# Kernel tuning notes

Hardware: AMD Instinct MI355X
Metric: run time of the kernel (lower is better)

The kernel has to match this reference:

```python
import jax, jax.numpy as jnp
import numpy as np

SPATIAL_SHAPES = np.array([[100, 100], [50, 50], [25, 25], [13, 13]], dtype=np.int32)
EMBED, NH, NL, NP = 256, 8, 4, 4
HD = EMBED // NH  # 32


def setup_inputs() -> dict:
    key = jax.random.key(0)
    ks = jax.random.split(key, 12)
    bs, nq = 4, 4000
    nv = int((SPATIAL_SHAPES[:, 0] * SPATIAL_SHAPES[:, 1]).sum())  # 13294
    s_lin = 1.0 / np.sqrt(EMBED)  # xavier-ish scale
    s_small = 0.02                # offsets/weights heads start near init
    return {
        "query": jax.random.normal(ks[0], (bs, nq, EMBED), jnp.float32),
        "value": jax.random.normal(ks[1], (bs, nv, EMBED), jnp.float32),
        "reference_points": jax.random.uniform(ks[2], (bs, nq, NL, 2), jnp.float32),
        "spatial_shapes": jnp.asarray(SPATIAL_SHAPES),
        "W_off": jax.random.normal(ks[3], (EMBED, NH * NL * NP * 2), jnp.float32) * s_small,
        "b_off": jax.random.normal(ks[4], (NH * NL * NP * 2,), jnp.float32) * s_small,
        "W_attn": jax.random.normal(ks[5], (EMBED, NH * NL * NP), jnp.float32) * s_small,
        "b_attn": jax.random.normal(ks[6], (NH * NL * NP,), jnp.float32) * s_small,
        "W_val": jax.random.normal(ks[7], (EMBED, EMBED), jnp.float32) * s_lin,
        "b_val": jnp.zeros((EMBED,), jnp.float32),
        "W_out": jax.random.normal(ks[8], (EMBED, EMBED), jnp.float32) * s_lin,
        "b_out": jnp.zeros((EMBED,), jnp.float32),
    }


def _bilinear_sample(val_l, H, W, x, y):
    """grid_sample(mode=bilinear, padding=zeros, align_corners=False) equivalent.
    val_l: [bs, nh, H*W, hd]; x, y: [bs, nh, nq, np] pixel-space coords.
    Returns [bs, nh, nq, np, hd]."""
    x0 = jnp.floor(x)
    y0 = jnp.floor(y)
    bs, nh, nq, npts = x.shape
    out = 0.0
    for dx, dy in ((0, 0), (1, 0), (0, 1), (1, 1)):
        xi = x0 + dx
        yi = y0 + dy
        w = (1.0 - jnp.abs(x - xi)) * (1.0 - jnp.abs(y - yi))
        valid = (xi >= 0) & (xi < W) & (yi >= 0) & (yi < H)
        idx = (jnp.clip(yi, 0, H - 1) * W + jnp.clip(xi, 0, W - 1)).astype(jnp.int32)
        g = jnp.take_along_axis(val_l, idx.reshape(bs, nh, nq * npts, 1), axis=2)
        g = g.reshape(bs, nh, nq, npts, -1)
        out = out + g * (w * valid.astype(w.dtype))[..., None]
    return out


def reference(query, value, reference_points, spatial_shapes,
              W_off, b_off, W_attn, b_attn, W_val, b_val, W_out, b_out):
    shapes = np.asarray(spatial_shapes)  # static level shapes
    bs, nq, _ = query.shape
    # value projection -> per-head layout [bs, nh, nv, hd]
    v = (value @ W_val + b_val).reshape(bs, -1, NH, HD).transpose(0, 2, 1, 3)
    # sampling offsets and attention weights from query
    off = (query @ W_off + b_off).reshape(bs, nq, NH, NL, NP, 2)
    attn = jax.nn.softmax((query @ W_attn + b_attn).reshape(bs, nq, NH, NL * NP), axis=-1)
    attn = attn.reshape(bs, nq, NH, NL, NP)
    # normalized sampling locations; normalizer = (W, H) per level
    normalizer = jnp.asarray(np.stack([shapes[:, 1], shapes[:, 0]], -1), jnp.float32)
    loc = reference_points[:, :, None, :, None, :] + off / normalizer[None, None, None, :, None, :]
    out = jnp.zeros((bs, NH, nq, HD), query.dtype)
    start = 0
    for l in range(NL):
        H, W = int(shapes[l, 0]), int(shapes[l, 1])
        val_l = v[:, :, start:start + H * W, :]
        # pixel coords with align_corners=False: p = loc*size - 0.5
        x = loc[:, :, :, l, :, 0].transpose(0, 2, 1, 3) * W - 0.5  # [bs,nh,nq,np]
        y = loc[:, :, :, l, :, 1].transpose(0, 2, 1, 3) * H - 0.5
        sampled = _bilinear_sample(val_l, H, W, x, y)  # [bs,nh,nq,np,hd]
        out = out + jnp.einsum('bhqpd,bqhp->bhqd', sampled, attn[:, :, :, l, :])
        start += H * W
    out = out.transpose(0, 2, 1, 3).reshape(bs, nq, EMBED)
    return out @ W_out + b_out
```

## Files before the change

### kernel.cpp

```cpp
#include <hip/hip_runtime.h>
#include <hip/hip_bf16.h>

#define EMBED 256
#define NH 8
#define NL 4
#define NP 4
#define HD 32
#define BS 4
#define NQ 4000
#define NV 13294

using f32x4   = __attribute__((ext_vector_type(4))) float;
using bf16x8  = __attribute__((ext_vector_type(8))) short;

__device__ __forceinline__ float bf2f_lo(unsigned u) {
    union { unsigned u; float f; } x; x.u = u << 16; return x.f;
}
__device__ __forceinline__ float bf2f_hi(unsigned u) {
    union { unsigned u; float f; } x; x.u = u & 0xffff0000u; return x.f;
}
__device__ __forceinline__ unsigned short f2bf(float f) {
    union { float f; unsigned u; } x; x.f = f;
    unsigned u = x.u;
    return (unsigned short)((u + 0x7fffu + ((u >> 16) & 1u)) >> 16);
}
__device__ __forceinline__ unsigned cvtpk(float lo, float hi) {
    unsigned r;
    asm("v_cvt_pk_bf16_f32 %0, %1, %2" : "=v"(r) : "v"(lo), "v"(hi));
    return r;
}

__device__ __forceinline__ void async16(const void* g, void* l) {
    __builtin_amdgcn_global_load_lds(
        (const __attribute__((address_space(1))) void*)g,
        (__attribute__((address_space(3))) void*)l, 16, 0, 0);
}

template<int N> __device__ __forceinline__ void wait_vmcnt() {
    if constexpr (N == 0)      asm volatile("s_waitcnt vmcnt(0)" ::: "memory");
    else if constexpr (N == 2) asm volatile("s_waitcnt vmcnt(2)" ::: "memory");
    else if constexpr (N == 3) asm volatile("s_waitcnt vmcnt(3)" ::: "memory");
}

__global__ __launch_bounds__(256) void msda_prep_k(
    const float* __restrict__ W_val, const float* __restrict__ W_out,
    const float* __restrict__ W_off, const float* __restrict__ W_attn,
    const float* __restrict__ b_off, const float* __restrict__ b_attn,
    unsigned short* __restrict__ Wt_val, unsigned short* __restrict__ Wt_out,
    unsigned short* __restrict__ Wt_qa, float* __restrict__ b_qa)
{
    int i = blockIdx.x * 256 + threadIdx.x;
    if (i < 384) b_qa[i] = (i < 256) ? b_off[i] : b_attn[i - 256];
    if (i < 65536) {
        int r = i >> 8, c = i & 255;
        Wt_val[c * 256 + r] = f2bf(W_val[i]);
    } else if (i < 131072) {
        int j = i - 65536, r = j >> 8, c = j & 255;
        Wt_out[c * 256 + r] = f2bf(W_out[j]);
    } else if (i < 229376) {
        int j = i - 131072;
        int n = j >> 8, k = j & 255;
        float v = (n < 256) ? W_off[k * 256 + n] : W_attn[k * 128 + (n - 256)];
        Wt_qa[j] = f2bf(v);
    }
}

template<int EPI, bool ABF16>
__device__ __forceinline__ void gemm_body(
    char* lds,
    const void* __restrict__ Ap,
    const unsigned short* __restrict__ Bt,
    const float* __restrict__ bias,
    void* __restrict__ out,
    int M, int N, int mblk, int nblk)
{
    constexpr int K = 256, C = 8;
    constexpr int NI = 2;
    constexpr int ABYTES = 128 * 32 * 2;
    constexpr int BUFB   = ABYTES + 128 * 32 * 2;
    constexpr int LOPS   = ABF16 ? 1 : 2;

    const int m0 = mblk * 128, n0 = nblk * 128;
    const int tid  = threadIdx.x;
    const int w    = tid >> 6;
    const int lane = tid & 63;
    const int quad = lane >> 4;
    const int l16  = lane & 15;
    const int wm   = (w & 1) * 64;
    const int wn   = (w >> 1) * 32;

    const int ar  = tid >> 2;
    const int arg = min(m0 + ar, M - 1);
    const int ak  = (tid & 3) * 8;
    const float*          afp = (const float*)Ap          + (size_t)arg * K + ak;
    const unsigned short* abp = (const unsigned short*)Ap + (size_t)arg * K + ak;

    const char* bgp = (const char*)(Bt + (size_t)(n0 + w * 16 + (lane >> 2)) * K)
                      + (lane & 3) * 16;

    auto issueB = [&](int c, int kb) {
        async16(bgp + c * 64, lds + kb * BUFB + ABYTES + w * 1024);
    };

    float4 aLoR[2], aHiR[2];
    bf16x8 aRegR[2];
    auto loadA = [&](int c) {
        const int p = c & 1;
        if constexpr (ABF16) {
            aRegR[p] = *(const bf16x8*)(abp + c * 32);
        } else {
            aLoR[p] = *(const float4*)(afp + c * 32);
            aHiR[p] = *(const float4*)(afp + c * 32 + 4);
        }
    };
    auto writeA = [&](int c) {
        const int p = c & 1;
        unsigned short* dst = (unsigned short*)(lds + (c % 3) * BUFB) + ar * 32 + ak;
        if constexpr (ABF16) {
            *(bf16x8*)dst = aRegR[p];
        } else {
            union { unsigned u[4]; bf16x8 v; } t;
            t.u[0] = cvtpk(aLoR[p].x, aLoR[p].y); t.u[1] = cvtpk(aLoR[p].z, aLoR[p].w);
            t.u[2] = cvtpk(aHiR[p].x, aHiR[p].y); t.u[3] = cvtpk(aHiR[p].z, aHiR[p].w);
            *(bf16x8*)dst = t.v;
        }
    };

    f32x4 acc[4][NI];
#pragma unroll
    for (int a = 0; a < 4; a++)
#pragma unroll
        for (int b = 0; b < NI; b++) acc[a][b] = (f32x4){0.f, 0.f, 0.f, 0.f};

    loadA(0); issueB(0, 0); loadA(1); issueB(1, 1);
    writeA(0);

#pragma unroll
    for (int c = 0; c < C; c++) {
        if (c < C - 1) wait_vmcnt<LOPS + 1>(); else wait_vmcnt<0>();
        asm volatile("s_waitcnt lgkmcnt(0)" ::: "memory");
        __builtin_amdgcn_s_barrier();
        __builtin_amdgcn_sched_barrier(0);
        if (c + 2 < C) { loadA(c + 2); issueB(c + 2, (c + 2) % 3); }

        const char* aL = lds + (c % 3) * BUFB;
        const char* bL = aL + ABYTES;
        bf16x8 af[4], bfr[NI];
#pragma unroll
        for (int mi = 0; mi < 4; mi++)
            af[mi] = *(const bf16x8*)(aL + (wm + mi * 16 + l16) * 64 + quad * 16);
#pragma unroll
        for (int ni = 0; ni < NI; ni++)
            bfr[ni] = *(const bf16x8*)(bL + (wn + ni * 16 + l16) * 64 + quad * 16);

        if (c + 1 < C) writeA(c + 1);

#pragma unroll
        for (int mi = 0; mi < 4; mi++)
#pragma unroll
            for (int ni = 0; ni < NI; ni++)
                acc[mi][ni] = __builtin_amdgcn_mfma_f32_16x16x32_bf16(af[mi], bfr[ni], acc[mi][ni], 0, 0, 0);
    }

    if constexpr (EPI == 0) {
        __syncthreads();
        unsigned short* cs = (unsigned short*)lds;
#pragma unroll
        for (int ni = 0; ni < NI; ni++) {
            int cl = wn + ni * 16 + l16;
            float bvv = bias[n0 + cl];
#pragma unroll
            for (int mi = 0; mi < 4; mi++)
#pragma unroll
                for (int r = 0; r < 4; r++) {
                    int ml = wm + mi * 16 + quad * 4 + r;
                    cs[ml * 136 + cl] = f2bf(acc[mi][ni][r] + bvv);
                }
        }
        __syncthreads();
        const int seg = tid >> 7, rr = tid & 127;
        const int m = m0 + rr;
        if (m < M) {
            const int b   = m / NV;
            const int pix = m - b * NV;
            const int h   = (n0 >> 5) + seg;
            char* dst = (char*)out + (((size_t)b * 8 + h) * NV + pix) * 64;
            const uint4* s = (const uint4*)&cs[rr * 136 + seg * 32];
#pragma unroll
            for (int j = 0; j < 4; j++) ((uint4*)dst)[j] = s[j];
        }
    } else {
#pragma unroll
        for (int ni = 0; ni < NI; ni++) {
            int cc = n0 + wn + ni * 16 + l16;
            float bvv = bias[cc];
#pragma unroll
            for (int mi = 0; mi < 4; mi++)
#pragma unroll
                for (int r = 0; r < 4; r++) {
                    int m = m0 + wm + mi * 16 + quad * 4 + r;
                    if (m >= M) continue;
                    ((float*)out)[(size_t)m * N + cc] = acc[mi][ni][r] + bvv;
                }
        }
    }
}

__global__ __launch_bounds__(512) void msda_gemm_vq_k(
    const float* __restrict__ value, const float* __restrict__ query,
    const unsigned short* __restrict__ Wt_val, const unsigned short* __restrict__ Wt_qa,
    const float* __restrict__ b_val, const float* __restrict__ b_qa,
    unsigned short* __restrict__ v_buf, float* __restrict__ oa_buf)
{
    extern __shared__ char lds[];
    const int bx = blockIdx.x;
    if (bx < 832) {
        gemm_body<0, false>(lds, value, Wt_val, b_val, v_buf,
                            BS * NV, 256, bx >> 1, bx & 1);
    } else {
        const int j = bx - 832;
        const int mb = j / 3;
        gemm_body<1, false>(lds, query, Wt_qa, b_qa, oa_buf,
                            BS * NQ, 384, mb, j - mb * 3);
    }
}

__global__ __launch_bounds__(512) void msda_gemm_out_k(
    const unsigned short* __restrict__ t_buf,
    const unsigned short* __restrict__ Wt_out,
    const float* __restrict__ b_out,
    float* __restrict__ out)
{
    extern __shared__ char lds[];
    const int bx = blockIdx.x;
    gemm_body<1, true>(lds, t_buf, Wt_out, b_out, out,
                       BS * NQ, 256, bx >> 1, bx & 1);
}

__global__ __launch_bounds__(256) void msda_sampler_k(
    const float* __restrict__ refpts,
    const float* __restrict__ oa_buf,
    const unsigned short* __restrict__ v_buf,
    unsigned short* __restrict__ t_out)
{
    __shared__ float  oa_s[4][384];
    __shared__ float  ref_s[4][8];
    __shared__ float4 wtab[528];
    __shared__ int2   itab[528];

    const int tid = threadIdx.x;
    const int q0  = blockIdx.x * 4;

    {
        const float4* src = (const float4*)(oa_buf + (size_t)q0 * 384);
        float4* dst = (float4*)&oa_s[0][0];
        dst[tid] = src[tid];
        if (tid < 128) dst[256 + tid] = src[256 + tid];
        if (tid < 32) ((float*)ref_s)[tid] = refpts[q0 * 8 + tid];
    }
    __syncthreads();

    const int HWs[4]    = {100, 50, 25, 13};
    const int starts[4] = {0, 10000, 12500, 13125};
#pragma unroll
    for (int it = 0; it < 2; it++) {
        int s  = tid + it * 256;
        int i  = s & 15;
        int h  = (s >> 4) & 7;
        int ql = s >> 7;
        int l  = i >> 2, p = i & 3;
        float logit = oa_s[ql][256 + h * 16 + i];
        float m = logit;
#pragma unroll
        for (int off = 1; off < 16; off <<= 1) m = fmaxf(m, __shfl_xor(m, off, 64));
        float e = __expf(logit - m);
        float sum = e;
#pragma unroll
        for (int off = 1; off < 16; off <<= 1) sum += __shfl_xor(sum, off, 64);
        float a = e / sum;

        int Wl = HWs[l];
        float fW = (float)Wl;
        float rx = ref_s[ql][l * 2], ry = ref_s[ql][l * 2 + 1];
        float offx = oa_s[ql][h * 32 + l * 8 + p * 2];
        float offy = oa_s[ql][h * 32 + l * 8 + p * 2 + 1];
        float x = rx * fW + offx - 0.5f;
        float y = ry * fW + offy - 0.5f;
        float xf = floorf(x), yf = floorf(y);
        float fx = x - xf, fy = y - yf;
        int x0 = (int)xf, y0 = (int)yf;
        int x1 = x0 + 1, y1 = y0 + 1;
        float wx0 = (x0 >= 0 && x0 < Wl) ? (1.f - fx) : 0.f;
        float wx1 = (x1 >= 0 && x1 < Wl) ? fx : 0.f;
        float wy0 = (y0 >= 0 && y0 < Wl) ? (1.f - fy) : 0.f;
        float wy1 = (y1 >= 0 && y1 < Wl) ? fy : 0.f;
        int x0c = min(max(x0, 0), Wl - 1), x1c = min(max(x1, 0), Wl - 1);
        int y0c = min(max(y0, 0), Wl - 1), y1c = min(max(y1, 0), Wl - 1);
        int r0 = starts[l] + y0c * Wl, r1 = starts[l] + y1c * Wl;

        int xb = min(max(x0, 0), Wl - 2);
        float wlo = ((x0c == xb)     ? wx0 : 0.f) + ((x1c == xb)     ? wx1 : 0.f);
        float whi = ((x0c == xb + 1) ? wx0 : 0.f) + ((x1c == xb + 1) ? wx1 : 0.f);

        int ti = i * 33 + ql * 8 + h;
        wtab[ti] = make_float4(wy0 * a, wy1 * a, wlo, whi);
        itab[ti] = make_int2(r0 + xb, r1 + xb);
    }
    __syncthreads();

    const int dg4 = tid & 3, xc = (tid >> 2) & 1, h = (tid >> 3) & 7, ql = tid >> 6;
    const int q = q0 + ql;
    const int b = q / NQ;
    const char* base = (const char*)v_buf + ((size_t)(b * 8 + h)) * NV * 64 + dg4 * 16;
    const int tbase = ql * 8 + h;

    float a0 = 0.f, a1 = 0.f, a2 = 0.f, a3 = 0.f;
    float a4 = 0.f, a5 = 0.f, a6 = 0.f, a7 = 0.f;
#pragma unroll
    for (int lp = 0; lp < 16; lp++) {
        float4 wv = wtab[lp * 33 + tbase];
        int2   iv = itab[lp * 33 + tbase];
        uint4 s0 = *(const uint4*)(base + ((unsigned)(iv.x + xc) << 6));
        uint4 s1 = *(const uint4*)(base + ((unsigned)(iv.y + xc) << 6));
        float wx = xc ? wv.w : wv.z;
        float w0 = wx * wv.x, w1 = wx * wv.y;
        a0 += w0 * bf2f_lo(s0.x); a1 += w0 * bf2f_hi(s0.x);
        a2 += w0 * bf2f_lo(s0.y); a3 += w0 * bf2f_hi(s0.y);
        a4 += w0 * bf2f_lo(s0.z); a5 += w0 * bf2f_hi(s0.z);
        a6 += w0 * bf2f_lo(s0.w); a7 += w0 * bf2f_hi(s0.w);
        a0 += w1 * bf2f_lo(s1.x); a1 += w1 * bf2f_hi(s1.x);
        a2 += w1 * bf2f_lo(s1.y); a3 += w1 * bf2f_hi(s1.y);
        a4 += w1 * bf2f_lo(s1.z); a5 += w1 * bf2f_hi(s1.z);
        a6 += w1 * bf2f_lo(s1.w); a7 += w1 * bf2f_hi(s1.w);
    }
    a0 += __shfl_xor(a0, 4, 64); a1 += __shfl_xor(a1, 4, 64);
    a2 += __shfl_xor(a2, 4, 64); a3 += __shfl_xor(a3, 4, 64);
    a4 += __shfl_xor(a4, 4, 64); a5 += __shfl_xor(a5, 4, 64);
    a6 += __shfl_xor(a6, 4, 64); a7 += __shfl_xor(a7, 4, 64);
    if (xc == 0) {
        uint4 o;
        o.x = (unsigned)f2bf(a0) | ((unsigned)f2bf(a1) << 16);
        o.y = (unsigned)f2bf(a2) | ((unsigned)f2bf(a3) << 16);
        o.z = (unsigned)f2bf(a4) | ((unsigned)f2bf(a5) << 16);
        o.w = (unsigned)f2bf(a6) | ((unsigned)f2bf(a7) << 16);
        *(uint4*)(t_out + (size_t)q * 256 + h * 32 + dg4 * 8) = o;
    }
}

extern "C" void kernel_launch(void* const* d_in, const int* in_sizes, int n_in,
                              void* d_out, int out_size, void* d_ws, size_t ws_size,
                              hipStream_t stream) {
    const float* query  = (const float*)d_in[0];
    const float* value  = (const float*)d_in[1];
    const float* refpts = (const float*)d_in[2];
    const float* W_off  = (const float*)d_in[4];
    const float* b_off  = (const float*)d_in[5];
    const float* W_attn = (const float*)d_in[6];
    const float* b_attn = (const float*)d_in[7];
    const float* W_val  = (const float*)d_in[8];
    const float* b_val  = (const float*)d_in[9];
    const float* W_out  = (const float*)d_in[10];
    const float* b_out  = (const float*)d_in[11];

    char* wsp = (char*)d_ws;
    size_t o = 0;
    auto carve = [&](size_t bytes) -> void* {
        void* p = wsp + o; o += (bytes + 255) & ~(size_t)255; return p;
    };
    unsigned short* Wt_val = (unsigned short*)carve(256 * 256 * 2);
    unsigned short* Wt_out = (unsigned short*)carve(256 * 256 * 2);
    unsigned short* Wt_qa  = (unsigned short*)carve(384 * 256 * 2);
    float*          b_qa   = (float*)carve(384 * 4);
    unsigned short* v_buf  = (unsigned short*)carve((size_t)BS * NH * NV * 32 * 2);
    float*          oa_buf = (float*)carve((size_t)BS * NQ * 384 * 4);
    unsigned short* t_buf  = (unsigned short*)carve((size_t)BS * NQ * EMBED * 2);

    msda_prep_k<<<896, 256, 0, stream>>>(W_val, W_out, W_off, W_attn,
                                         b_off, b_attn, Wt_val, Wt_out, Wt_qa, b_qa);

    msda_gemm_vq_k<<<832 + 375, 512, 49152, stream>>>(value, query, Wt_val, Wt_qa,
                                                      b_val, b_qa, v_buf, oa_buf);
    msda_sampler_k<<<(BS * NQ) / 4, 256, 0, stream>>>(refpts, oa_buf, v_buf, t_buf);
    msda_gemm_out_k<<<250, 512, 49152, stream>>>(t_buf, Wt_out, b_out, (float*)d_out);
}
```

Baseline: 193.6 us.

## Use smaller 64x64 tiles for output GEMM and XCD-chunked block remap

Replaces the output-projection GEMM with a dedicated kernel that uses 64x64 tiles, 256 threads and a three-stage LDS ring. This raises the grid from 250 to 1000 blocks so all CUs on the chip get work. It also remaps block indices in the value/query GEMM so that consecutive logical tiles land on the same XCD, which should improve L2 locality. Smaller tiles reload more operand data per output and keep the pipeline shallow.

```diff
diff --git a/kernel.cpp b/kernel.cpp
--- a/kernel.cpp
+++ b/kernel.cpp
@@ -40,6 +40,12 @@
     if constexpr (N == 0)      asm volatile("s_waitcnt vmcnt(0)" ::: "memory");
     else if constexpr (N == 2) asm volatile("s_waitcnt vmcnt(2)" ::: "memory");
     else if constexpr (N == 3) asm volatile("s_waitcnt vmcnt(3)" ::: "memory");
+}
+
+__device__ __forceinline__ int xcd_chunk(int s, int nwg) {
+    const int q = nwg >> 3, r = nwg & 7;
+    const int x = s & 7, i = s >> 3;
+    return (x < r ? x * (q + 1) : r * (q + 1) + (x - r) * q) + i;
 }
 
 __global__ __launch_bounds__(256) void msda_prep_k(
@@ -213,7 +219,7 @@
     unsigned short* __restrict__ v_buf, float* __restrict__ oa_buf)
 {
     extern __shared__ char lds[];
-    const int bx = blockIdx.x;
+    const int bx = xcd_chunk(blockIdx.x, 832 + 375);
     if (bx < 832) {
         gemm_body<0, false>(lds, value, Wt_val, b_val, v_buf,
                             BS * NV, 256, bx >> 1, bx & 1);
@@ -225,16 +231,80 @@
     }
 }
 
-__global__ __launch_bounds__(512) void msda_gemm_out_k(
+__global__ __launch_bounds__(256) void msda_gemm_out_k(
     const unsigned short* __restrict__ t_buf,
     const unsigned short* __restrict__ Wt_out,
     const float* __restrict__ b_out,
     float* __restrict__ out)
 {
     extern __shared__ char lds[];
+    constexpr int K = 256, C = 8, M = BS * NQ, N = 256;
+    constexpr int ABYTES = 64 * 32 * 2;
+    constexpr int BUFB   = ABYTES + 64 * 32 * 2;
     const int bx = blockIdx.x;
-    gemm_body<1, true>(lds, t_buf, Wt_out, b_out, out,
-                       BS * NQ, 256, bx >> 1, bx & 1);
+    const int m0 = (bx >> 2) * 64, n0 = (bx & 3) * 64;
+    const int tid  = threadIdx.x;
+    const int w    = tid >> 6;
+    const int lane = tid & 63;
+    const int quad = lane >> 4;
+    const int l16  = lane & 15;
+    const int wn   = w * 16;
+
+    const int ar  = tid >> 2;
+    const int ak  = (tid & 3) * 8;
+    const unsigned short* abp = t_buf + (size_t)(m0 + ar) * K + ak;
+
+    const char* bgp = (const char*)(Wt_out + (size_t)(n0 + w * 16 + (lane >> 2)) * K)
+                      + (lane & 3) * 16;
+    auto issueB = [&](int c, int kb) {
+        async16(bgp + c * 64, lds + kb * BUFB + ABYTES + w * 1024);
+    };
+
+    bf16x8 aRegR[2];
+    auto loadA  = [&](int c) { aRegR[c & 1] = *(const bf16x8*)(abp + c * 32); };
+    auto writeA = [&](int c) {
+        *(bf16x8*)((unsigned short*)(lds + (c % 3) * BUFB) + ar * 32 + ak) = aRegR[c & 1];
+    };
+
+    f32x4 acc[4];
+#pragma unroll
+    for (int a = 0; a < 4; a++) acc[a] = (f32x4){0.f, 0.f, 0.f, 0.f};
+
+    loadA(0); issueB(0, 0); loadA(1); issueB(1, 1);
+    writeA(0);
+
+#pragma unroll
+    for (int c = 0; c < C; c++) {
+        if (c < C - 1) wait_vmcnt<2>(); else wait_vmcnt<0>();
+        asm volatile("s_waitcnt lgkmcnt(0)" ::: "memory");
+        __builtin_amdgcn_s_barrier();
+        __builtin_amdgcn_sched_barrier(0);
+        if (c + 2 < C) { loadA(c + 2); issueB(c + 2, (c + 2) % 3); }
+
+        const char* aL = lds + (c % 3) * BUFB;
+        const char* bL = aL + ABYTES;
+        bf16x8 af[4], bfr;
+#pragma unroll
+        for (int mi = 0; mi < 4; mi++)
+            af[mi] = *(const bf16x8*)(aL + (mi * 16 + l16) * 64 + quad * 16);
+        bfr = *(const bf16x8*)(bL + (wn + l16) * 64 + quad * 16);
+
+        if (c + 1 < C) writeA(c + 1);
+
+#pragma unroll
+        for (int mi = 0; mi < 4; mi++)
+            acc[mi] = __builtin_amdgcn_mfma_f32_16x16x32_bf16(af[mi], bfr, acc[mi], 0, 0, 0);
+    }
+
+    const int cc = n0 + wn + l16;
+    const float bvv = b_out[cc];
+#pragma unroll
+    for (int mi = 0; mi < 4; mi++)
+#pragma unroll
+        for (int r = 0; r < 4; r++) {
+            int m = m0 + mi * 16 + quad * 4 + r;
+            out[(size_t)m * N + cc] = acc[mi][r] + bvv;
+        }
 }
 
 __global__ __launch_bounds__(256) void msda_sampler_k(
@@ -381,5 +451,5 @@
     msda_gemm_vq_k<<<832 + 375, 512, 49152, stream>>>(value, query, Wt_val, Wt_qa,
                                                       b_val, b_qa, v_buf, oa_buf);
     msda_sampler_k<<<(BS * NQ) / 4, 256, 0, stream>>>(refpts, oa_buf, v_buf, t_buf);
-    msda_gemm_out_k<<<250, 512, 49152, stream>>>(t_buf, Wt_out, b_out, (float*)d_out);
-}
+    msda_gemm_out_k<<<1000, 256, 24576, stream>>>(t_buf, Wt_out, b_out, (float*)d_out);
+}
```

Result: slower. 200.4 us (+3.5%).

## Fuse deformable sampler with output projection GEMM via LDS-staged tile

Applied to the files above, without the earlier changes.

Merges the sampling kernel and the output projection GEMM into one kernel. Each block processes 16 queries in four sub-batches of 4, stages the bf16 sampled features in shared memory, and then runs a 16x256 MFMA GEMM against Wt_out read directly from global memory. This removes the t_buf round trip and one kernel launch. In exchange, each block re-reads the whole Wt_out matrix (only cached, not tiled), there is less parallelism per block, and extra barriers serialize the sub-batches.

```diff
diff --git a/kernel.cpp b/kernel.cpp
--- a/kernel.cpp
+++ b/kernel.cpp
@@ -225,125 +225,153 @@
     }
 }
 
-__global__ __launch_bounds__(512) void msda_gemm_out_k(
-    const unsigned short* __restrict__ t_buf,
+__global__ __launch_bounds__(256) void msda_sampout_k(
+    const float* __restrict__ refpts,
+    const float* __restrict__ oa_buf,
+    const unsigned short* __restrict__ v_buf,
     const unsigned short* __restrict__ Wt_out,
     const float* __restrict__ b_out,
     float* __restrict__ out)
-{
-    extern __shared__ char lds[];
-    const int bx = blockIdx.x;
-    gemm_body<1, true>(lds, t_buf, Wt_out, b_out, out,
-                       BS * NQ, 256, bx >> 1, bx & 1);
-}
-
-__global__ __launch_bounds__(256) void msda_sampler_k(
-    const float* __restrict__ refpts,
-    const float* __restrict__ oa_buf,
-    const unsigned short* __restrict__ v_buf,
-    unsigned short* __restrict__ t_out)
 {
     __shared__ float  oa_s[4][384];
     __shared__ float  ref_s[4][8];
     __shared__ float4 wtab[528];
     __shared__ int2   itab[528];
+    __shared__ unsigned short t_s[16][288];
 
     const int tid = threadIdx.x;
-    const int q0  = blockIdx.x * 4;
-
-    {
-        const float4* src = (const float4*)(oa_buf + (size_t)q0 * 384);
-        float4* dst = (float4*)&oa_s[0][0];
-        dst[tid] = src[tid];
-        if (tid < 128) dst[256 + tid] = src[256 + tid];
-        if (tid < 32) ((float*)ref_s)[tid] = refpts[q0 * 8 + tid];
-    }
-    __syncthreads();
+    const int q0  = blockIdx.x * 16;
+    const int b   = q0 / NQ;
 
     const int HWs[4]    = {100, 50, 25, 13};
     const int starts[4] = {0, 10000, 12500, 13125};
-#pragma unroll
-    for (int it = 0; it < 2; it++) {
-        int s  = tid + it * 256;
-        int i  = s & 15;
-        int h  = (s >> 4) & 7;
-        int ql = s >> 7;
-        int l  = i >> 2, p = i & 3;
-        float logit = oa_s[ql][256 + h * 16 + i];
-        float m = logit;
-#pragma unroll
-        for (int off = 1; off < 16; off <<= 1) m = fmaxf(m, __shfl_xor(m, off, 64));
-        float e = __expf(logit - m);
-        float sum = e;
-#pragma unroll
-        for (int off = 1; off < 16; off <<= 1) sum += __shfl_xor(sum, off, 64);
-        float a = e / sum;
-
-        int Wl = HWs[l];
-        float fW = (float)Wl;
-        float rx = ref_s[ql][l * 2], ry = ref_s[ql][l * 2 + 1];
-        float offx = oa_s[ql][h * 32 + l * 8 + p * 2];
-        float offy = oa_s[ql][h * 32 + l * 8 + p * 2 + 1];
-        float x = rx * fW + offx - 0.5f;
-        float y = ry * fW + offy - 0.5f;
-        float xf = floorf(x), yf = floorf(y);
-        float fx = x - xf, fy = y - yf;
-        int x0 = (int)xf, y0 = (int)yf;
-        int x1 = x0 + 1, y1 = y0 + 1;
-        float wx0 = (x0 >= 0 && x0 < Wl) ? (1.f - fx) : 0.f;
-        float wx1 = (x1 >= 0 && x1 < Wl) ? fx : 0.f;
-        float wy0 = (y0 >= 0 && y0 < Wl) ? (1.f - fy) : 0.f;
-        float wy1 = (y1 >= 0 && y1 < Wl) ? fy : 0.f;
-        int x0c = min(max(x0, 0), Wl - 1), x1c = min(max(x1, 0), Wl - 1);
-        int y0c = min(max(y0, 0), Wl - 1), y1c = min(max(y1, 0), Wl - 1);
-        int r0 = starts[l] + y0c * Wl, r1 = starts[l] + y1c * Wl;
-
-        int xb = min(max(x0, 0), Wl - 2);
-        float wlo = ((x0c == xb)     ? wx0 : 0.f) + ((x1c == xb)     ? wx1 : 0.f);
-        float whi = ((x0c == xb + 1) ? wx0 : 0.f) + ((x1c == xb + 1) ? wx1 : 0.f);
-
-        int ti = i * 33 + ql * 8 + h;
-        wtab[ti] = make_float4(wy0 * a, wy1 * a, wlo, whi);
-        itab[ti] = make_int2(r0 + xb, r1 + xb);
+
+    for (int sb = 0; sb < 4; sb++) {
+        const int qb = q0 + sb * 4;
+        __syncthreads();
+        {
+            const float4* src = (const float4*)(oa_buf + (size_t)qb * 384);
+            float4* dst = (float4*)&oa_s[0][0];
+            dst[tid] = src[tid];
+            if (tid < 128) dst[256 + tid] = src[256 + tid];
+            if (tid < 32) ((float*)ref_s)[tid] = refpts[qb * 8 + tid];
+        }
+        __syncthreads();
+
+#pragma unroll
+        for (int it = 0; it < 2; it++) {
+            int s  = tid + it * 256;
+            int i  = s & 15;
+            int h  = (s >> 4) & 7;
+            int ql = s >> 7;
+            int l  = i >> 2, p = i & 3;
+            float logit = oa_s[ql][256 + h * 16 + i];
+            float m = logit;
+#pragma unroll
+            for (int off = 1; off < 16; off <<= 1) m = fmaxf(m, __shfl_xor(m, off, 64));
+            float e = __expf(logit - m);
+            float sum = e;
+#pragma unroll
+            for (int off = 1; off < 16; off <<= 1) sum += __shfl_xor(sum, off, 64);
+            float a = e / sum;
+
+            int Wl = HWs[l];
+            float fW = (float)Wl;
+            float rx = ref_s[ql][l * 2], ry = ref_s[ql][l * 2 + 1];
+            float offx = oa_s[ql][h * 32 + l * 8 + p * 2];
+            float offy = oa_s[ql][h * 32 + l * 8 + p * 2 + 1];
+            float x = rx * fW + offx - 0.5f;
+            float y = ry * fW + offy - 0.5f;
+            float xf = floorf(x), yf = floorf(y);
+            float fx = x - xf, fy = y - yf;
+            int x0 = (int)xf, y0 = (int)yf;
+            int x1 = x0 + 1, y1 = y0 + 1;
+            float wx0 = (x0 >= 0 && x0 < Wl) ? (1.f - fx) : 0.f;
+            float wx1 = (x1 >= 0 && x1 < Wl) ? fx : 0.f;
+            float wy0 = (y0 >= 0 && y0 < Wl) ? (1.f - fy) : 0.f;
+            float wy1 = (y1 >= 0 && y1 < Wl) ? fy : 0.f;
+            int x0c = min(max(x0, 0), Wl - 1), x1c = min(max(x1, 0), Wl - 1);
+            int y0c = min(max(y0, 0), Wl - 1), y1c = min(max(y1, 0), Wl - 1);
+            int r0 = starts[l] + y0c * Wl, r1 = starts[l] + y1c * Wl;
+
+            int xb = min(max(x0, 0), Wl - 2);
+            float wlo = ((x0c == xb)     ? wx0 : 0.f) + ((x1c == xb)     ? wx1 : 0.f);
+            float whi = ((x0c == xb + 1) ? wx0 : 0.f) + ((x1c == xb + 1) ? wx1 : 0.f);
+
+            int ti = i * 33 + ql * 8 + h;
+            wtab[ti] = make_float4(wy0 * a, wy1 * a, wlo, whi);
+            itab[ti] = make_int2(r0 + xb, r1 + xb);
+        }
+        __syncthreads();
+
+        const int dg4 = tid & 3, xc = (tid >> 2) & 1, h = (tid >> 3) & 7, ql = tid >> 6;
+        const char* base = (const char*)v_buf + ((size_t)(b * 8 + h)) * NV * 64 + dg4 * 16;
+        const int tbase = ql * 8 + h;
+
+        float a0 = 0.f, a1 = 0.f, a2 = 0.f, a3 = 0.f;
+        float a4 = 0.f, a5 = 0.f, a6 = 0.f, a7 = 0.f;
+#pragma unroll
+        for (int lp = 0; lp < 16; lp++) {
+            float4 wv = wtab[lp * 33 + tbase];
+            int2   iv = itab[lp * 33 + tbase];
+            uint4 s0 = *(const uint4*)(base + ((unsigned)(iv.x + xc) << 6));
+            uint4 s1 = *(const uint4*)(base + ((unsigned)(iv.y + xc) << 6));
+            float wx = xc ? wv.w : wv.z;
+            float w0 = wx * wv.x, w1 = wx * wv.y;
+            a0 += w0 * bf2f_lo(s0.x); a1 += w0 * bf2f_hi(s0.x);
+            a2 += w0 * bf2f_lo(s0.y); a3 += w0 * bf2f_hi(s0.y);
+            a4 += w0 * bf2f_lo(s0.z); a5 += w0 * bf2f_hi(s0.z);
+            a6 += w0 * bf2f_lo(s0.w); a7 += w0 * bf2f_hi(s0.w);
+            a0 += w1 * bf2f_lo(s1.x); a1 += w1 * bf2f_hi(s1.x);
+            a2 += w1 * bf2f_lo(s1.y); a3 += w1 * bf2f_hi(s1.y);
+            a4 += w1 * bf2f_lo(s1.z); a5 += w1 * bf2f_hi(s1.z);
+            a6 += w1 * bf2f_lo(s1.w); a7 += w1 * bf2f_hi(s1.w);
+        }
+        a0 += __shfl_xor(a0, 4, 64); a1 += __shfl_xor(a1, 4, 64);
+        a2 += __shfl_xor(a2, 4, 64); a3 += __shfl_xor(a3, 4, 64);
+        a4 += __shfl_xor(a4, 4, 64); a5 += __shfl_xor(a5, 4, 64);
+        a6 += __shfl_xor(a6, 4, 64); a7 += __shfl_xor(a7, 4, 64);
+        if (xc == 0) {
+            uint4 o;
+            o.x = (unsigned)f2bf(a0) | ((unsigned)f2bf(a1) << 16);
+            o.y = (unsigned)f2bf(a2) | ((unsigned)f2bf(a3) << 16);
+            o.z = (unsigned)f2bf(a4) | ((unsigned)f2bf(a5) << 16);
+            o.w = (unsigned)f2bf(a6) | ((unsigned)f2bf(a7) << 16);
+            *(uint4*)&t_s[sb * 4 + ql][h * 32 + dg4 * 8] = o;
+        }
     }
     __syncthreads();
 
-    const int dg4 = tid & 3, xc = (tid >> 2) & 1, h = (tid >> 3) & 7, ql = tid >> 6;
-    const int q = q0 + ql;
-    const int b = q / NQ;
-    const char* base = (const char*)v_buf + ((size_t)(b * 8 + h)) * NV * 64 + dg4 * 16;
-    const int tbase = ql * 8 + h;
-
-    float a0 = 0.f, a1 = 0.f, a2 = 0.f, a3 = 0.f;
-    float a4 = 0.f, a5 = 0.f, a6 = 0.f, a7 = 0.f;
-#pragma unroll
-    for (int lp = 0; lp < 16; lp++) {
-        float4 wv = wtab[lp * 33 + tbase];
-        int2   iv = itab[lp * 33 + tbase];
-        uint4 s0 = *(const uint4*)(base + ((unsigned)(iv.x + xc) << 6));
-        uint4 s1 = *(const uint4*)(base + ((unsigned)(iv.y + xc) << 6));
-        float wx = xc ? wv.w : wv.z;
-        float w0 = wx * wv.x, w1 = wx * wv.y;
-        a0 += w0 * bf2f_lo(s0.x); a1 += w0 * bf2f_hi(s0.x);
-        a2 += w0 * bf2f_lo(s0.y); a3 += w0 * bf2f_hi(s0.y);
-        a4 += w0 * bf2f_lo(s0.z); a5 += w0 * bf2f_hi(s0.z);
-        a6 += w0 * bf2f_lo(s0.w); a7 += w0 * bf2f_hi(s0.w);
-        a0 += w1 * bf2f_lo(s1.x); a1 += w1 * bf2f_hi(s1.x);
-        a2 += w1 * bf2f_lo(s1.y); a3 += w1 * bf2f_hi(s1.y);
-        a4 += w1 * bf2f_lo(s1.z); a5 += w1 * bf2f_hi(s1.z);
-        a6 += w1 * bf2f_lo(s1.w); a7 += w1 * bf2f_hi(s1.w);
-    }
-    a0 += __shfl_xor(a0, 4, 64); a1 += __shfl_xor(a1, 4, 64);
-    a2 += __shfl_xor(a2, 4, 64); a3 += __shfl_xor(a3, 4, 64);
-    a4 += __shfl_xor(a4, 4, 64); a5 += __shfl_xor(a5, 4, 64);
-    a6 += __shfl_xor(a6, 4, 64); a7 += __shfl_xor(a7, 4, 64);
-    if (xc == 0) {
-        uint4 o;
-        o.x = (unsigned)f2bf(a0) | ((unsigned)f2bf(a1) << 16);
-        o.y = (unsigned)f2bf(a2) | ((unsigned)f2bf(a3) << 16);
-        o.z = (unsigned)f2bf(a4) | ((unsigned)f2bf(a5) << 16);
-        o.w = (unsigned)f2bf(a6) | ((unsigned)f2bf(a7) << 16);
-        *(uint4*)(t_out + (size_t)q * 256 + h * 32 + dg4 * 8) = o;
+    const int w    = tid >> 6;
+    const int lane = tid & 63;
+    const int quad = lane >> 4;
+    const int l16  = lane & 15;
+    const int wn   = w * 64;
+
+    f32x4 acc[4];
+#pragma unroll
+    for (int a = 0; a < 4; a++) acc[a] = (f32x4){0.f, 0.f, 0.f, 0.f};
+
+#pragma unroll
+    for (int c = 0; c < 8; c++) {
+        bf16x8 af = *(const bf16x8*)&t_s[l16][c * 32 + quad * 8];
+#pragma unroll
+        for (int ni = 0; ni < 4; ni++) {
+            bf16x8 bfr = *(const bf16x8*)(Wt_out + (size_t)(wn + ni * 16 + l16) * 256
+                                          + c * 32 + quad * 8);
+            acc[ni] = __builtin_amdgcn_mfma_f32_16x16x32_bf16(af, bfr, acc[ni], 0, 0, 0);
+        }
+    }
+
+#pragma unroll
+    for (int ni = 0; ni < 4; ni++) {
+        const int cc = wn + ni * 16 + l16;
+        const float bvv = b_out[cc];
+#pragma unroll
+        for (int r = 0; r < 4; r++) {
+            const int m = q0 + quad * 4 + r;
+            out[(size_t)m * 256 + cc] = acc[ni][r] + bvv;
+        }
     }
 }
 
@@ -373,13 +401,12 @@
     float*          b_qa   = (float*)carve(384 * 4);
     unsigned short* v_buf  = (unsigned short*)carve((size_t)BS * NH * NV * 32 * 2);
     float*          oa_buf = (float*)carve((size_t)BS * NQ * 384 * 4);
-    unsigned short* t_buf  = (unsigned short*)carve((size_t)BS * NQ * EMBED * 2);
 
     msda_prep_k<<<896, 256, 0, stream>>>(W_val, W_out, W_off, W_attn,
                                          b_off, b_attn, Wt_val, Wt_out, Wt_qa, b_qa);
 
     msda_gemm_vq_k<<<832 + 375, 512, 49152, stream>>>(value, query, Wt_val, Wt_qa,
                                                       b_val, b_qa, v_buf, oa_buf);
-    msda_sampler_k<<<(BS * NQ) / 4, 256, 0, stream>>>(refpts, oa_buf, v_buf, t_buf);
-    msda_gemm_out_k<<<250, 512, 49152, stream>>>(t_buf, Wt_out, b_out, (float*)d_out);
-}
+    msda_sampout_k<<<(BS * NQ) / 16, 256, 0, stream>>>(refpts, oa_buf, v_buf,
+                                                       Wt_out, b_out, (float*)d_out);
+}
```

New measurement: 196.1 us. About the same (+1.3%).
